# Performance work log

Hardware: AMD Instinct MI355X
Metric: run time of the kernel (lower is better)

## Reference

```python
import jax, jax.numpy as jnp
import numpy as np
import math

NUM_CLASSES = 722
BLUR_RANGE = 3
# gaussian_val(dist, sigma=1) = exp(-2**dist / (2 * 2**1)) = exp(-2**dist / 4)
DECAYS = [math.exp(-(2.0 ** d) / 4.0) for d in range(BLUR_RANGE + 1)]


def setup_inputs() -> dict:
    key = jax.random.key(0)
    k1, k2 = jax.random.split(key)
    pred = jax.random.normal(k1, (32, 2048, NUM_CLASSES), dtype=jnp.float32)
    target = jax.random.randint(k2, (32, 2048), 0, NUM_CLASSES, dtype=jnp.int32)
    return {"pred": pred, "target": target}


def _smoothed_label(target):
    # target: (b, t) int -> (b, t, C) float32 gaussian-blurred one-hot.
    b, t = target.shape
    bi = jnp.arange(b)[:, None]   # (b, 1)
    ti = jnp.arange(t)[None, :]   # (1, t)
    one_hot = jnp.zeros((b, t, NUM_CLASSES), dtype=jnp.float32)
    # Same scatter order as the torch loop: dist = blur..0, direction +1 then -1;
    # later (smaller-dist) scatters overwrite earlier ones, incl. clamped indices.
    for dist in range(BLUR_RANGE, -1, -1):
        for direction in (1, -1):
            blur_idx = jnp.clip(target + direction * dist, 0, NUM_CLASSES - 1)
            one_hot = one_hot.at[bi, ti, blur_idx].set(DECAYS[dist])
    # to_onehot: exact target position gets 1.0 (overwrites decay[0]).
    one_hot = one_hot.at[bi, ti, target].set(1.0)
    return one_hot


def reference(pred, target):
    # pred: (b, t, C) logits; target: (b, t) class indices.
    pred_logit = jax.nn.log_softmax(pred, axis=-1)
    target_smoothed = _smoothed_label(target)
    target_loss_sum = jnp.sum(-pred_logit * target_smoothed, axis=-1)  # (b, t)
    return jnp.mean(target_loss_sum)
```

## Files before the change

### kernel.cpp

```cpp
#include <hip/hip_runtime.h>
#include <math.h>

#define NC 722
#define NROWS 65536
#define PAIRS_PER_WAVE 4
#define ROWS_PER_WAVE 8
#define WAVES_PER_BLOCK 4
#define ROWS_PER_BLOCK 32
#define NF4 361

__global__ void init_out_kernel(float* out) {
    if (threadIdx.x == 0) out[0] = 0.0f;
}

__global__ __launch_bounds__(256) void ce_gauss_kernel(
        const float* __restrict__ pred,
        const int* __restrict__ target,
        float* __restrict__ out) {
    const int lane = threadIdx.x & 63;
    const int wave = threadIdx.x >> 6;

    __shared__ float wt_lds[WAVES_PER_BLOCK][ROWS_PER_WAVE * 8];
    __shared__ float se_lds[WAVES_PER_BLOCK][ROWS_PER_WAVE];
    __shared__ int   tg_lds[WAVES_PER_BLOCK][ROWS_PER_WAVE];
    __shared__ float wave_sums[WAVES_PER_BLOCK];

    const int row0 = blockIdx.x * ROWS_PER_BLOCK + wave * ROWS_PER_WAVE;

    const float4* __restrict__ p4[PAIRS_PER_WAVE];
    #pragma unroll
    for (int p = 0; p < PAIRS_PER_WAVE; ++p)
        p4[p] = (const float4*)(pred + (size_t)(row0 + 2 * p) * NC);

    float se[ROWS_PER_WAVE] = {0.f, 0.f, 0.f, 0.f, 0.f, 0.f, 0.f, 0.f};
    #pragma unroll
    for (int k = 0; k < 6; ++k) {
        const int g = lane + (k << 6);
        if (g < NF4) {
            const bool aE = (g < 180);
            const bool aO = (g > 180);
            #pragma unroll
            for (int p = 0; p < PAIRS_PER_WAVE; ++p) {
                float4 v = p4[p][g];
                float e0 = __expf(v.x), e1 = __expf(v.y);
                float e2 = __expf(v.z), e3 = __expf(v.w);
                float s01 = e0 + e1, s23 = e2 + e3, s4 = s01 + s23;
                se[2 * p]     += aE ? s4 : (aO ? 0.f : s01);
                se[2 * p + 1] += aO ? s4 : (aE ? 0.f : s23);
            }
        }
    }

    {
        const float DEC1 = 0.606530659713f;
        const float DEC2 = 0.367879441171f;
        const float DEC3 = 0.135335283237f;
        #pragma unroll
        for (int rr = 0; rr < ROWS_PER_WAVE; ++rr) {
            const int t = target[row0 + rr];
            float w[7] = {0.f, 0.f, 0.f, 0.f, 0.f, 0.f, 0.f};
            #pragma unroll
            for (int dist = 3; dist >= 1; --dist) {
                const float dv = (dist == 3) ? DEC3 : (dist == 2) ? DEC2 : DEC1;
                int ip = t + dist; if (ip > NC - 1) ip = NC - 1;
                int im = t - dist; if (im < 0) im = 0;
                w[ip - t + 3] = dv;
                w[im - t + 3] = dv;
            }
            w[3] = 1.0f;
            const float sw = w[0] + w[1] + w[2] + w[3] + w[4] + w[5] + w[6];
            if (lane == 0) {
                #pragma unroll
                for (int j = 0; j < 7; ++j) wt_lds[wave][rr * 8 + j] = w[j];
                wt_lds[wave][rr * 8 + 7] = sw;
                tg_lds[wave][rr] = t;
            }
        }
    }

    #pragma unroll
    for (int rr = 0; rr < ROWS_PER_WAVE; ++rr) {
        #pragma unroll
        for (int off = 32; off > 0; off >>= 1)
            se[rr] += __shfl_xor(se[rr], off, 64);
    }
    if (lane == 0) {
        #pragma unroll
        for (int rr = 0; rr < ROWS_PER_WAVE; ++rr) se_lds[wave][rr] = se[rr];
    }

    const int grr = lane >> 3;
    const int gj  = lane & 7;
    const int t   = tg_lds[wave][grr];
    float dotv = 0.f;
    if (gj < 7) {
        const float wv = wt_lds[wave][grr * 8 + gj];
        if (wv > 0.f) {
            dotv = wv * pred[(size_t)(row0 + grr) * NC + (t - 3 + gj)];
        }
    }
    dotv += __shfl_xor(dotv, 1, 64);
    dotv += __shfl_xor(dotv, 2, 64);
    dotv += __shfl_xor(dotv, 4, 64);

    float acc = 0.f;
    if (gj == 0) {
        const float sw  = wt_lds[wave][grr * 8 + 7];
        const float sev = se_lds[wave][grr];
        acc = sw * __logf(sev) - dotv;
    }
    #pragma unroll
    for (int off = 32; off > 0; off >>= 1)
        acc += __shfl_xor(acc, off, 64);

    if (lane == 0) wave_sums[wave] = acc;
    __syncthreads();
    if (threadIdx.x == 0) {
        float s = wave_sums[0] + wave_sums[1] + wave_sums[2] + wave_sums[3];
        atomicAdd(out, s * (1.0f / (float)NROWS));
    }
}

extern "C" void kernel_launch(void* const* d_in, const int* in_sizes, int n_in,
                              void* d_out, int out_size, void* d_ws, size_t ws_size,
                              hipStream_t stream) {
    const float* pred = (const float*)d_in[0];
    const int* target = (const int*)d_in[1];
    float* out = (float*)d_out;

    init_out_kernel<<<1, 64, 0, stream>>>(out);

    const int grid = NROWS / ROWS_PER_BLOCK;
    ce_gauss_kernel<<<grid, 256, 0, stream>>>(pred, target, out);
}
```

Measured before the change: 286.3 us.

## Load rows as float2 with all loads issued upfront, halve rows per wave

Replaces the paired-row float4 loads (which needed per-lane masking at the row boundary) with per-row float2 loads. All loads for a wave's four rows are now issued into registers before the target/weight setup and the exp-sum pass, with out-of-range lanes clamped instead of branched. Rows per block drop from 32 to 16, doubling the grid. The aim is more memory-level parallelism per wave and simpler indexing, at the cost of narrower loads and higher register use.

Result: faster. 261.5 us (-8.6%).

```diff
diff --git a/kernel.cpp b/kernel.cpp
--- a/kernel.cpp
+++ b/kernel.cpp
@@ -2,12 +2,12 @@
 #include <math.h>
 
 #define NC 722
+#define NF2 361
 #define NROWS 65536
-#define PAIRS_PER_WAVE 4
-#define ROWS_PER_WAVE 8
+#define ROWS_PER_WAVE 4
 #define WAVES_PER_BLOCK 4
-#define ROWS_PER_BLOCK 32
-#define NF4 361
+#define ROWS_PER_BLOCK 16
+#define KITERS 6
 
 __global__ void init_out_kernel(float* out) {
     if (threadIdx.x == 0) out[0] = 0.0f;
@@ -27,28 +27,19 @@
 
     const int row0 = blockIdx.x * ROWS_PER_BLOCK + wave * ROWS_PER_WAVE;
 
-    const float4* __restrict__ p4[PAIRS_PER_WAVE];
+    const float2* __restrict__ p2[ROWS_PER_WAVE];
     #pragma unroll
-    for (int p = 0; p < PAIRS_PER_WAVE; ++p)
-        p4[p] = (const float4*)(pred + (size_t)(row0 + 2 * p) * NC);
+    for (int rr = 0; rr < ROWS_PER_WAVE; ++rr)
+        p2[rr] = (const float2*)(pred + (size_t)(row0 + rr) * NC);
 
-    float se[ROWS_PER_WAVE] = {0.f, 0.f, 0.f, 0.f, 0.f, 0.f, 0.f, 0.f};
+    float2 v[ROWS_PER_WAVE][KITERS];
     #pragma unroll
-    for (int k = 0; k < 6; ++k) {
-        const int g = lane + (k << 6);
-        if (g < NF4) {
-            const bool aE = (g < 180);
-            const bool aO = (g > 180);
-            #pragma unroll
-            for (int p = 0; p < PAIRS_PER_WAVE; ++p) {
-                float4 v = p4[p][g];
-                float e0 = __expf(v.x), e1 = __expf(v.y);
-                float e2 = __expf(v.z), e3 = __expf(v.w);
-                float s01 = e0 + e1, s23 = e2 + e3, s4 = s01 + s23;
-                se[2 * p]     += aE ? s4 : (aO ? 0.f : s01);
-                se[2 * p + 1] += aO ? s4 : (aE ? 0.f : s23);
-            }
-        }
+    for (int k = 0; k < KITERS; ++k) {
+        int idx = lane + (k << 6);
+        if (idx > NF2 - 1) idx = NF2 - 1;
+        #pragma unroll
+        for (int rr = 0; rr < ROWS_PER_WAVE; ++rr)
+            v[rr][k] = p2[rr][idx];
     }
 
     {
@@ -78,6 +69,17 @@
         }
     }
 
+    float se[ROWS_PER_WAVE] = {0.f, 0.f, 0.f, 0.f};
+    #pragma unroll
+    for (int k = 0; k < KITERS; ++k) {
+        const bool valid = (k < KITERS - 1) || (lane < NF2 - 5 * 64);
+        #pragma unroll
+        for (int rr = 0; rr < ROWS_PER_WAVE; ++rr) {
+            const float s = __expf(v[rr][k].x) + __expf(v[rr][k].y);
+            se[rr] += valid ? s : 0.f;
+        }
+    }
+
     #pragma unroll
     for (int rr = 0; rr < ROWS_PER_WAVE; ++rr) {
         #pragma unroll
@@ -91,9 +93,9 @@
 
     const int grr = lane >> 3;
     const int gj  = lane & 7;
-    const int t   = tg_lds[wave][grr];
     float dotv = 0.f;
-    if (gj < 7) {
+    if (grr < ROWS_PER_WAVE && gj < 7) {
+        const int t = tg_lds[wave][grr];
         const float wv = wt_lds[wave][grr * 8 + gj];
         if (wv > 0.f) {
             dotv = wv * pred[(size_t)(row0 + grr) * NC + (t - 3 + gj)];
@@ -104,7 +106,7 @@
     dotv += __shfl_xor(dotv, 4, 64);
 
     float acc = 0.f;
-    if (gj == 0) {
+    if (gj == 0 && grr < ROWS_PER_WAVE) {
         const float sw  = wt_lds[wave][grr * 8 + 7];
         const float sev = se_lds[wave][grr];
         acc = sw * __logf(sev) - dotv;
```
